# Performance work log

Hardware: AMD Instinct MI355X
Metric: run time of the kernel (lower is better)

The kernel has to match this reference:

```python
import jax, jax.numpy as jnp
import numpy as np

N_EMBED = 2048
NUM_EXPERTS = 64
TOP_K = 8
B, S = 4, 4096


def setup_inputs() -> dict:
    key = jax.random.key(0)
    k_x, k_n, k_w1, k_b1, k_w2, k_b2 = jax.random.split(key, 6)
    bound = 1.0 / np.sqrt(N_EMBED)  # torch nn.Linear default init range
    return {
        "x": jax.random.normal(k_x, (B, S, N_EMBED), dtype=jnp.float32),
        "noise": jax.random.normal(k_n, (B, S, NUM_EXPERTS), dtype=jnp.float32),
        "W1": jax.random.uniform(k_w1, (N_EMBED, NUM_EXPERTS), jnp.float32, -bound, bound),
        "b1": jax.random.uniform(k_b1, (NUM_EXPERTS,), jnp.float32, -bound, bound),
        "W2": jax.random.uniform(k_w2, (N_EMBED, NUM_EXPERTS), jnp.float32, -bound, bound),
        "b2": jax.random.uniform(k_b2, (NUM_EXPERTS,), jnp.float32, -bound, bound),
    }


def reference(x, noise, W1, b1, W2, b2):
    # logits = lin1(x); noise_scale = softplus(lin2(x))
    logits = jnp.einsum("bsd,de->bse", x, W1) + b1          # [B,S,E]
    scale = jax.nn.softplus(jnp.einsum("bsd,de->bse", x, W2) + b2)
    mixed = logits + noise * scale                            # [B,S,E]
    full = jax.nn.softmax(mixed, axis=-1)

    topk_vals, topk_idx = jax.lax.top_k(mixed, TOP_K)         # [B,S,K]

    # scatter topk values into a -inf background, then softmax (masked softmax)
    E = mixed.shape[-1]
    flat_mixed = mixed.reshape(-1, E)
    flat_idx = topk_idx.reshape(-1, TOP_K)
    flat_vals = topk_vals.reshape(-1, TOP_K)
    rows = jnp.arange(flat_mixed.shape[0])[:, None]
    sparse = jnp.full_like(flat_mixed, -jnp.inf).at[rows, flat_idx].set(flat_vals)
    sparse_sm = jax.nn.softmax(sparse, axis=-1).reshape(mixed.shape)

    return sparse_sm, topk_idx, full
```

## Files before the change

kernel.cpp:

```cpp
#include <hip/hip_runtime.h>
#include <math.h>


typedef _Float16 f16x8 __attribute__((ext_vector_type(8)));
typedef _Float16 f16x4 __attribute__((ext_vector_type(4)));
typedef float f32x4 __attribute__((ext_vector_type(4)));

constexpr int ND = 2048, NE = 64, NK = 8, NTOK = 16384;
constexpr int KC   = 32;
constexpr int NCHT = ND / KC;
constexpr int CPSG = 4;
constexpr int NSTG = NCHT / CPSG;
constexpr int HSTG = NSTG / 2;
constexpr int MTOK = 32;
constexpr int ZROW = 132;
constexpr int STG_F16 = CPSG * MTOK * 64;

__global__ void prep_w(const float* __restrict__ W1, const float* __restrict__ W2,
                       _Float16* __restrict__ wt3) {
    const int g    = blockIdx.x * 256 + threadIdx.x;
    const int cg   = g >> 9;
    const int rem  = g & 511;
    const int t    = rem >> 6;
    const int lane = rem & 63;
    const int col  = lane & 15, q = lane >> 4;
    const int n    = t * 16 + col;
    const float* W = (t < 4) ? W1 : W2;
    const int cn   = n & 63;
    _Float16 h[8], l[8];
    #pragma unroll
    for (int j = 0; j < 8; ++j) {
        const float v = W[(size_t)(cg * 32 + q * 8 + j) * 64 + cn];
        const _Float16 hh = (_Float16)v;
        h[j] = hh;
        l[j] = (_Float16)((v - (float)hh) * 2048.0f);
    }
    *(f16x8*)&wt3[((size_t)(cg * 2 + 0) * 8 + t) * 512 + lane * 8] = *(f16x8*)h;
    *(f16x8*)&wt3[((size_t)(cg * 2 + 1) * 8 + t) * 512 + lane * 8] = *(f16x8*)l;
}

__device__ __forceinline__ void split4(const float4 v, f16x4& hh, f16x4& ll) {
    const _Float16 h0 = (_Float16)v.x, h1 = (_Float16)v.y,
                   h2 = (_Float16)v.z, h3 = (_Float16)v.w;
    hh = (f16x4){h0, h1, h2, h3};
    ll = (f16x4){(_Float16)((v.x - (float)h0) * 2048.0f),
                 (_Float16)((v.y - (float)h1) * 2048.0f),
                 (_Float16)((v.z - (float)h2) * 2048.0f),
                 (_Float16)((v.w - (float)h3) * 2048.0f)};
}

__device__ __forceinline__ void block_sync_lds() {
    asm volatile("s_waitcnt lgkmcnt(0)" ::: "memory");
    __builtin_amdgcn_s_barrier();
}

__global__ __launch_bounds__(256, 2)
void router_fused(const float* __restrict__ x, const _Float16* __restrict__ wt3,
                  const float* __restrict__ noise,
                  const float* __restrict__ b1, const float* __restrict__ b2,
                  float* __restrict__ out_sparse, float* __restrict__ out_idx,
                  float* __restrict__ out_full) {
    __shared__ __align__(16) _Float16 stage[2][STG_F16];
    const int tid  = threadIdx.x;
    const int lane = tid & 63;
    const int wu   = __builtin_amdgcn_readfirstlane(tid >> 6);
    const int col  = lane & 15, q = lane >> 4;
    const long tok0 = (long)blockIdx.x * MTOK;
    const int ta = 2 * wu, tb = 2 * wu + 1;

    const int stok = tid >> 3, lsub = tid & 7;
    const float* xs = x + (tok0 + stok) * (size_t)ND + lsub * 4;
    const int wS = lsub >> 1, wh = lsub & 1;

    const _Float16* wla = wt3 + (size_t)ta * 512 + (size_t)lane * 8;
    const _Float16* wlb = wt3 + (size_t)tb * 512 + (size_t)lane * 8;

    f32x4 a0[2][2], a1[2][2], zk0[2][2];
    #pragma unroll
    for (int m = 0; m < 2; ++m)
        #pragma unroll
        for (int i = 0; i < 2; ++i)
            #pragma unroll
            for (int r = 0; r < 4; ++r) { a0[m][i][r] = 0.f; a1[m][i][r] = 0.f; }

    f16x8 Ba[CPSG][4], Bb[CPSG][4];
    float4 xa[4], xb[4];

    auto loadB = [&](f16x8 (&B)[CPSG][4], const int s) {
        #pragma unroll
        for (int cc = 0; cc < CPSG; ++cc) {
            const size_t cb = (size_t)(s * CPSG + cc) * 8192;
            B[cc][0] = *(const f16x8*)(wla + cb);
            B[cc][1] = *(const f16x8*)(wlb + cb);
            B[cc][2] = *(const f16x8*)(wla + cb + 4096);
            B[cc][3] = *(const f16x8*)(wlb + cb + 4096);
        }
    };
    auto loadX = [&](float4 (&xr)[4], const int s) {
        #pragma unroll
        for (int j = 0; j < 4; ++j)
            xr[j] = *(const float4*)(xs + (size_t)s * 128 + (size_t)j * KC);
    };
    auto deposit = [&](_Float16* wb, const float4 (&xr)[4]) {
        #pragma unroll
        for (int j = 0; j < 4; ++j) {
            f16x4 hv, lv; split4(xr[j], hv, lv);
            const int idx = ((j * MTOK + stok) << 6)
                          + (((wS ^ (stok & 7) ^ ((j & 1) << 2)) << 3) + (wh << 2));
            *(f16x4*)&wb[idx]      = hv;
            *(f16x4*)&wb[idx ^ 32] = lv;
        }
    };

    auto do_stage = [&](const int s, const _Float16* rb, _Float16* wb,
                        const f16x8 (&Bcur)[CPSG][4], f16x8 (&Bnxt)[CPSG][4],
                        const float4 (&xw)[4], float4 (&xl)[4]) {
        if (s + 1 < NSTG) loadB(Bnxt, s + 1);
        if (s + 2 < NSTG) loadX(xl, s + 2);
        #pragma unroll
        for (int cc = 0; cc < CPSG; ++cc) {
            const int swz = (cc & 1) << 2;
            #pragma unroll
            for (int mt = 0; mt < 2; ++mt) {
                const int ridx = ((cc * MTOK + mt * 16 + col) << 6)
                               + ((q ^ (col & 7) ^ swz) << 3);
                const f16x8 ah = *(const f16x8*)&rb[ridx];
                const f16x8 al = *(const f16x8*)&rb[ridx ^ 32];
                a0[mt][0] = __builtin_amdgcn_mfma_f32_16x16x32_f16(ah, Bcur[cc][0], a0[mt][0], 0, 0, 0);
                a0[mt][1] = __builtin_amdgcn_mfma_f32_16x16x32_f16(ah, Bcur[cc][1], a0[mt][1], 0, 0, 0);
                a1[mt][0] = __builtin_amdgcn_mfma_f32_16x16x32_f16(ah, Bcur[cc][2], a1[mt][0], 0, 0, 0);
                a1[mt][1] = __builtin_amdgcn_mfma_f32_16x16x32_f16(ah, Bcur[cc][3], a1[mt][1], 0, 0, 0);
                a1[mt][0] = __builtin_amdgcn_mfma_f32_16x16x32_f16(al, Bcur[cc][0], a1[mt][0], 0, 0, 0);
                a1[mt][1] = __builtin_amdgcn_mfma_f32_16x16x32_f16(al, Bcur[cc][1], a1[mt][1], 0, 0, 0);
            }
        }
        if (s == HSTG - 1) {
            #pragma unroll
            for (int m = 0; m < 2; ++m)
                #pragma unroll
                for (int i = 0; i < 2; ++i) {
                    zk0[m][i] = a0[m][i] + a1[m][i] * 4.8828125e-4f;
                    #pragma unroll
                    for (int r = 0; r < 4; ++r) { a0[m][i][r] = 0.f; a1[m][i][r] = 0.f; }
                }
        }
        if (s + 1 < NSTG) deposit(wb, xw);
        block_sync_lds();
    };

    {
        float4 x0[4];
        loadX(x0, 0);
        deposit(stage[0], x0);
        loadB(Ba, 0);
        loadX(xa, 1);
    }
    block_sync_lds();

    for (int sp = 0; sp < NSTG; sp += 2) {
        do_stage(sp,     stage[0], stage[1], Ba, Bb, xa, xb);
        do_stage(sp + 1, stage[1], stage[0], Bb, Ba, xb, xa);
    }

    float* zs = (float*)&stage[0][0];
    #pragma unroll
    for (int m = 0; m < 2; ++m)
        #pragma unroll
        for (int i = 0; i < 2; ++i) {
            const int n = (ta + i) * 16 + col;
            #pragma unroll
            for (int r = 0; r < 4; ++r) {
                const float zk1 = a0[m][i][r] + a1[m][i][r] * 4.8828125e-4f;
                const float comb = (float)((double)zk0[m][i][r] + (double)zk1);
                zs[(m * 16 + q * 4 + r) * ZROW + n] = comb;
            }
        }
    __syncthreads();

    const float b1v = b1[lane];
    const float b2v = b2[lane];
    for (int tt = 0; tt < 8; ++tt) {
        const int lt = wu * 8 + tt;
        const long tok = tok0 + lt;
        const float z1 = zs[lt * ZROW + lane] + b1v;
        const float z2 = zs[lt * ZROW + 64 + lane] + b2v;
        const float sc = (float)log1p(exp((double)z2));
        const float nz = noise[tok * NE + lane];
        const float mixed = z1 + nz * sc;

        float vmax = mixed;
        for (int off = 32; off; off >>= 1) vmax = fmaxf(vmax, __shfl_xor(vmax, off));
        const float e = expf(mixed - vmax);
        float denom = e;
        for (int off = 32; off; off >>= 1) denom += __shfl_xor(denom, off);
        const float fullv = e / denom;

        float cur = mixed;
        int   sel = 0;
        float myidxf = 0.0f;
        #pragma unroll
        for (int r = 0; r < NK; ++r) {
            float bv = cur; int bi = lane;
            for (int off = 32; off; off >>= 1) {
                const float ov = __shfl_xor(bv, off);
                const int   oi = __shfl_xor(bi, off);
                if (ov > bv || (ov == bv && oi < bi)) { bv = ov; bi = oi; }
            }
            if (lane == r)  myidxf = (float)bi;
            if (lane == bi) { sel = 1; cur = -INFINITY; }
        }

        const float es = sel ? e : 0.0f;
        float dsum = es;
        for (int off = 32; off; off >>= 1) dsum += __shfl_xor(dsum, off);
        const float sparsev = sel ? (e / dsum) : 0.0f;

        out_full[tok * NE + lane]   = fullv;
        out_sparse[tok * NE + lane] = sparsev;
        if (lane < NK) out_idx[tok * NK + lane] = myidxf;
    }
}

extern "C" void kernel_launch(void* const* d_in, const int* in_sizes, int n_in,
                              void* d_out, int out_size, void* d_ws, size_t ws_size,
                              hipStream_t stream) {
    const float* x     = (const float*)d_in[0];
    const float* noise = (const float*)d_in[1];
    const float* W1    = (const float*)d_in[2];
    const float* b1    = (const float*)d_in[3];
    const float* W2    = (const float*)d_in[4];
    const float* b2    = (const float*)d_in[5];

    float* out_sparse = (float*)d_out;
    float* out_idx    = out_sparse + (size_t)NTOK * NE;
    float* out_full   = out_idx + (size_t)NTOK * NK;

    _Float16* wt3 = (_Float16*)d_ws;

    prep_w<<<128, 256, 0, stream>>>(W1, W2, wt3);
    router_fused<<<NTOK / MTOK, 256, 0, stream>>>(x, wt3, noise, b1, b2,
                                                  out_sparse, out_idx, out_full);
}
```

Measured before the change: 255.9 us.

## Halve tokens per block and drop register prefetch to raise occupancy

Each block now handles 16 tokens instead of 32, with one M-tile per wave, and the launch bound asks for 4 blocks per CU instead of 2. The cross-stage register double-buffering of weight fragments and x prefetch is removed: weights are loaded at the start of each stage and x is prefetched only one stage ahead. The aim is to cut register pressure and raise occupancy, so latency is hidden by more waves rather than by software pipelining. In exchange, each weight fragment is reused across half as many tokens, which doubles total weight traffic from cache, and the loads are now less overlapped within each wave.

```diff
diff --git a/kernel.cpp b/kernel.cpp
--- a/kernel.cpp
+++ b/kernel.cpp
@@ -12,7 +12,7 @@
 constexpr int CPSG = 4;
 constexpr int NSTG = NCHT / CPSG;
 constexpr int HSTG = NSTG / 2;
-constexpr int MTOK = 32;
+constexpr int MTOK = 16;
 constexpr int ZROW = 132;
 constexpr int STG_F16 = CPSG * MTOK * 64;
 
@@ -54,7 +54,7 @@
     __builtin_amdgcn_s_barrier();
 }
 
-__global__ __launch_bounds__(256, 2)
+__global__ __launch_bounds__(256, 4)
 void router_fused(const float* __restrict__ x, const _Float16* __restrict__ wt3,
                   const float* __restrict__ noise,
                   const float* __restrict__ b1, const float* __restrict__ b2,
@@ -68,119 +68,112 @@
     const long tok0 = (long)blockIdx.x * MTOK;
     const int ta = 2 * wu, tb = 2 * wu + 1;
 
-    const int stok = tid >> 3, lsub = tid & 7;
-    const float* xs = x + (tok0 + stok) * (size_t)ND + lsub * 4;
-    const int wS = lsub >> 1, wh = lsub & 1;
+    const int stok = tid >> 4, fsub = tid & 15;
+    const float* xs = x + (tok0 + stok) * (size_t)ND + fsub * 4;
+    const int g8 = fsub & 7;
+    const int wS = g8 >> 1, wh = g8 & 1;
 
     const _Float16* wla = wt3 + (size_t)ta * 512 + (size_t)lane * 8;
     const _Float16* wlb = wt3 + (size_t)tb * 512 + (size_t)lane * 8;
 
-    f32x4 a0[2][2], a1[2][2], zk0[2][2];
+    f32x4 a0[2], a1[2], zk0[2];
     #pragma unroll
-    for (int m = 0; m < 2; ++m)
-        #pragma unroll
-        for (int i = 0; i < 2; ++i)
-            #pragma unroll
-            for (int r = 0; r < 4; ++r) { a0[m][i][r] = 0.f; a1[m][i][r] = 0.f; }
-
-    f16x8 Ba[CPSG][4], Bb[CPSG][4];
-    float4 xa[4], xb[4];
-
-    auto loadB = [&](f16x8 (&B)[CPSG][4], const int s) {
-        #pragma unroll
-        for (int cc = 0; cc < CPSG; ++cc) {
+    for (int i = 0; i < 2; ++i)
+        #pragma unroll
+        for (int r = 0; r < 4; ++r) { a0[i][r] = 0.f; a1[i][r] = 0.f; }
+
+    auto loadX = [&](float4 (&xr)[2], const int s) {
+        #pragma unroll
+        for (int j = 0; j < 2; ++j)
+            xr[j] = *(const float4*)(xs + (size_t)s * 128 + (size_t)j * 64);
+    };
+    auto deposit = [&](_Float16* wb, const float4 (&xr)[2]) {
+        #pragma unroll
+        for (int j = 0; j < 2; ++j) {
+            const int cc = j * 2 + (fsub >> 3);
+            f16x4 hv, lv; split4(xr[j], hv, lv);
+            const int idx = ((cc * MTOK + stok) << 6)
+                          + (((wS ^ (stok & 7) ^ ((cc & 1) << 2)) << 3) + (wh << 2));
+            *(f16x4*)&wb[idx]      = hv;
+            *(f16x4*)&wb[idx ^ 32] = lv;
+        }
+    };
+
+    auto do_stage = [&](const int s, const _Float16* rb, _Float16* wb) {
+        f16x8 B[CPSG][4];
+        #pragma unroll
+        for (int cc = 0; cc < 2; ++cc) {
             const size_t cb = (size_t)(s * CPSG + cc) * 8192;
             B[cc][0] = *(const f16x8*)(wla + cb);
             B[cc][1] = *(const f16x8*)(wlb + cb);
             B[cc][2] = *(const f16x8*)(wla + cb + 4096);
             B[cc][3] = *(const f16x8*)(wlb + cb + 4096);
         }
-    };
-    auto loadX = [&](float4 (&xr)[4], const int s) {
-        #pragma unroll
-        for (int j = 0; j < 4; ++j)
-            xr[j] = *(const float4*)(xs + (size_t)s * 128 + (size_t)j * KC);
-    };
-    auto deposit = [&](_Float16* wb, const float4 (&xr)[4]) {
-        #pragma unroll
-        for (int j = 0; j < 4; ++j) {
-            f16x4 hv, lv; split4(xr[j], hv, lv);
-            const int idx = ((j * MTOK + stok) << 6)
-                          + (((wS ^ (stok & 7) ^ ((j & 1) << 2)) << 3) + (wh << 2));
-            *(f16x4*)&wb[idx]      = hv;
-            *(f16x4*)&wb[idx ^ 32] = lv;
-        }
-    };
-
-    auto do_stage = [&](const int s, const _Float16* rb, _Float16* wb,
-                        const f16x8 (&Bcur)[CPSG][4], f16x8 (&Bnxt)[CPSG][4],
-                        const float4 (&xw)[4], float4 (&xl)[4]) {
-        if (s + 1 < NSTG) loadB(Bnxt, s + 1);
-        if (s + 2 < NSTG) loadX(xl, s + 2);
+        #pragma unroll
+        for (int cc = 2; cc < CPSG; ++cc) {
+            const size_t cb = (size_t)(s * CPSG + cc) * 8192;
+            B[cc][0] = *(const f16x8*)(wla + cb);
+            B[cc][1] = *(const f16x8*)(wlb + cb);
+            B[cc][2] = *(const f16x8*)(wla + cb + 4096);
+            B[cc][3] = *(const f16x8*)(wlb + cb + 4096);
+        }
+        float4 xl[2];
+        if (s + 1 < NSTG) loadX(xl, s + 1);
         #pragma unroll
         for (int cc = 0; cc < CPSG; ++cc) {
             const int swz = (cc & 1) << 2;
-            #pragma unroll
-            for (int mt = 0; mt < 2; ++mt) {
-                const int ridx = ((cc * MTOK + mt * 16 + col) << 6)
-                               + ((q ^ (col & 7) ^ swz) << 3);
-                const f16x8 ah = *(const f16x8*)&rb[ridx];
-                const f16x8 al = *(const f16x8*)&rb[ridx ^ 32];
-                a0[mt][0] = __builtin_amdgcn_mfma_f32_16x16x32_f16(ah, Bcur[cc][0], a0[mt][0], 0, 0, 0);
-                a0[mt][1] = __builtin_amdgcn_mfma_f32_16x16x32_f16(ah, Bcur[cc][1], a0[mt][1], 0, 0, 0);
-                a1[mt][0] = __builtin_amdgcn_mfma_f32_16x16x32_f16(ah, Bcur[cc][2], a1[mt][0], 0, 0, 0);
-                a1[mt][1] = __builtin_amdgcn_mfma_f32_16x16x32_f16(ah, Bcur[cc][3], a1[mt][1], 0, 0, 0);
-                a1[mt][0] = __builtin_amdgcn_mfma_f32_16x16x32_f16(al, Bcur[cc][0], a1[mt][0], 0, 0, 0);
-                a1[mt][1] = __builtin_amdgcn_mfma_f32_16x16x32_f16(al, Bcur[cc][1], a1[mt][1], 0, 0, 0);
-            }
+            const int ridx = ((cc * MTOK + col) << 6)
+                           + ((q ^ (col & 7) ^ swz) << 3);
+            const f16x8 ah = *(const f16x8*)&rb[ridx];
+            const f16x8 al = *(const f16x8*)&rb[ridx ^ 32];
+            a0[0] = __builtin_amdgcn_mfma_f32_16x16x32_f16(ah, B[cc][0], a0[0], 0, 0, 0);
+            a0[1] = __builtin_amdgcn_mfma_f32_16x16x32_f16(ah, B[cc][1], a0[1], 0, 0, 0);
+            a1[0] = __builtin_amdgcn_mfma_f32_16x16x32_f16(ah, B[cc][2], a1[0], 0, 0, 0);
+            a1[1] = __builtin_amdgcn_mfma_f32_16x16x32_f16(ah, B[cc][3], a1[1], 0, 0, 0);
+            a1[0] = __builtin_amdgcn_mfma_f32_16x16x32_f16(al, B[cc][0], a1[0], 0, 0, 0);
+            a1[1] = __builtin_amdgcn_mfma_f32_16x16x32_f16(al, B[cc][1], a1[1], 0, 0, 0);
         }
         if (s == HSTG - 1) {
             #pragma unroll
-            for (int m = 0; m < 2; ++m)
+            for (int i = 0; i < 2; ++i) {
+                zk0[i] = a0[i] + a1[i] * 4.8828125e-4f;
                 #pragma unroll
-                for (int i = 0; i < 2; ++i) {
-                    zk0[m][i] = a0[m][i] + a1[m][i] * 4.8828125e-4f;
-                    #pragma unroll
-                    for (int r = 0; r < 4; ++r) { a0[m][i][r] = 0.f; a1[m][i][r] = 0.f; }
-                }
-        }
-        if (s + 1 < NSTG) deposit(wb, xw);
+                for (int r = 0; r < 4; ++r) { a0[i][r] = 0.f; a1[i][r] = 0.f; }
+            }
+        }
+        if (s + 1 < NSTG) deposit(wb, xl);
         block_sync_lds();
     };
 
     {
-        float4 x0[4];
+        float4 x0[2];
         loadX(x0, 0);
         deposit(stage[0], x0);
-        loadB(Ba, 0);
-        loadX(xa, 1);
     }
     block_sync_lds();
 
     for (int sp = 0; sp < NSTG; sp += 2) {
-        do_stage(sp,     stage[0], stage[1], Ba, Bb, xa, xb);
-        do_stage(sp + 1, stage[1], stage[0], Bb, Ba, xb, xa);
+        do_stage(sp,     stage[0], stage[1]);
+        do_stage(sp + 1, stage[1], stage[0]);
     }
 
     float* zs = (float*)&stage[0][0];
     #pragma unroll
-    for (int m = 0; m < 2; ++m)
-        #pragma unroll
-        for (int i = 0; i < 2; ++i) {
-            const int n = (ta + i) * 16 + col;
-            #pragma unroll
-            for (int r = 0; r < 4; ++r) {
-                const float zk1 = a0[m][i][r] + a1[m][i][r] * 4.8828125e-4f;
-                const float comb = (float)((double)zk0[m][i][r] + (double)zk1);
-                zs[(m * 16 + q * 4 + r) * ZROW + n] = comb;
-            }
-        }
+    for (int i = 0; i < 2; ++i) {
+        const int n = (ta + i) * 16 + col;
+        #pragma unroll
+        for (int r = 0; r < 4; ++r) {
+            const float zk1 = a0[i][r] + a1[i][r] * 4.8828125e-4f;
+            const float comb = (float)((double)zk0[i][r] + (double)zk1);
+            zs[(q * 4 + r) * ZROW + n] = comb;
+        }
+    }
     __syncthreads();
 
     const float b1v = b1[lane];
     const float b2v = b2[lane];
-    for (int tt = 0; tt < 8; ++tt) {
-        const int lt = wu * 8 + tt;
+    for (int tt = 0; tt < 4; ++tt) {
+        const int lt = wu * 4 + tt;
         const long tok = tok0 + lt;
         const float z1 = zs[lt * ZROW + lane] + b1v;
         const float z2 = zs[lt * ZROW + 64 + lane] + b2v;
```

After: 249.6 us. 1.03x faster.
